# Performance work log

Measured on AMD Instinct MI355X. Metric: run time of the kernel, lower is better.

The kernel has to match this reference:

```python
import jax, jax.numpy as jnp
import numpy as np


def setup_inputs() -> dict:
    key = jax.random.key(0)
    k1, k2 = jax.random.split(key)
    B, S, H, T = 32, 524288, 512, 100
    n_frames = S // H  # 1024
    wrapped_phase = jax.random.uniform(k1, (B, S), dtype=jnp.float32)  # in [0,1)
    tables = jax.random.normal(k2, (B, n_frames + 1, T), dtype=jnp.float32)
    return {"wrapped_phase": wrapped_phase, "tables": tables, "hop_length": H}


def reference(wrapped_phase, tables, hop_length):
    # wrapped_phase: (B, S) in [0,1]; tables: (B, n_frames+1, T); hop_length: python int
    B, S = wrapped_phase.shape
    H = hop_length
    pad = (-S) % H
    wp = jnp.pad(wrapped_phase, ((0, 0), (0, pad)), mode="edge")
    wp = wp.reshape(B, -1, H)          # (B, F, H)
    Fr = wp.shape[1]
    if tables.shape[1] < Fr + 1:
        tables = jnp.pad(tables, ((0, 0), (0, Fr + 1 - tables.shape[1]), (0, 0)), mode="edge")
    else:
        tables = tables[:, : Fr + 1]
    L = tables.shape[2]
    # bilinear interp along table axis
    raw = wp * L                                   # (B, F, H)
    floor = jnp.clip(raw.astype(jnp.int32), 0, L - 1)
    p = raw - floor.astype(wp.dtype)
    # wrap-around pad: append first table entry at the end
    padded = jnp.concatenate([tables, tables[:, :, :1]], axis=2)  # (B, F+1, L+1)
    floor_flow = padded[:, :-1]   # table at frame start
    ceil_flow = padded[:, 1:]     # table at next frame

    def gather(t, idx):
        return jnp.take_along_axis(t, idx, axis=2)  # (B, F, H)

    v_floor = gather(floor_flow, floor) * (1.0 - p) + gather(floor_flow, floor + 1) * p
    v_ceil = gather(ceil_flow, floor) * (1.0 - p) + gather(ceil_flow, floor + 1) * p
    # lerp across hop-time
    p2 = jnp.arange(H, dtype=wp.dtype) / H          # (H,)
    final = v_floor * (1.0 - p2) + v_ceil * p2      # (B, F, H)
    return final.reshape(B, -1)[:, :S]
```

## Files before the change

### kernel.cpp

```cpp
#include <hip/hip_runtime.h>

constexpr int Bc  = 32;
constexpr int Sc  = 524288;
constexpr int Hc  = 512;
constexpr int Tc  = 100;
constexpr int FRc = Sc / Hc;
constexpr int FPB = 2;
constexpr int THREADS = 256;

typedef float floatx4 __attribute__((ext_vector_type(4)));

__global__ __launch_bounds__(THREADS) void gft_kernel(
    const float* __restrict__ wp,
    const float* __restrict__ tables,
    float* __restrict__ out)
{
    __shared__ floatx4 pk[FPB][Tc];

    const int blk = blockIdx.x;
    const int b   = blk >> 9;
    const int fp  = blk & 511;
    const int f   = fp * FPB;
    const int t   = threadIdx.x;

    const size_t base = (size_t)b * Sc + (size_t)fp * (FPB * Hc) + (size_t)t * 4;
    const floatx4 w = __builtin_nontemporal_load(
        reinterpret_cast<const floatx4*>(wp + base));

    const float* trow = tables + ((size_t)b * (FRc + 1) + (size_t)f) * Tc;
    if (t < FPB * Tc) {
        const int fr = (t >= Tc) ? 1 : 0;
        const int i  = t - fr * Tc;
        const int i1 = (i == Tc - 1) ? 0 : i + 1;
        const float* F = trow + fr * Tc;
        const float* C = F + Tc;
        floatx4 v;
        v.x = F[i]; v.y = F[i1]; v.z = C[i]; v.w = C[i1];
        pk[fr][i] = v;
    }
    __syncthreads();

    const int fi = t >> 7;
    const int h0 = (t & 127) * 4;

    const float wv[4] = {w.x, w.y, w.z, w.w};
    float r[4];
    #pragma unroll
    for (int j = 0; j < 4; ++j) {
        float raw = wv[j] * (float)Tc;
        int   fl  = (int)raw;
        fl = fl < 0 ? 0 : (fl > Tc - 1 ? Tc - 1 : fl);
        float p   = raw - (float)fl;
        float omp = 1.0f - p;
        floatx4 g = pk[fi][fl];
        float vf  = g.x * omp + g.y * p;
        float vc  = g.z * omp + g.w * p;
        float p2  = (float)(h0 + j) * (1.0f / (float)Hc);
        r[j] = vf * (1.0f - p2) + vc * p2;
    }
    floatx4 res;
    res.x = r[0]; res.y = r[1]; res.z = r[2]; res.w = r[3];
    __builtin_nontemporal_store(res, reinterpret_cast<floatx4*>(out + base));
}

extern "C" void kernel_launch(void* const* d_in, const int* in_sizes, int n_in,
                              void* d_out, int out_size, void* d_ws, size_t ws_size,
                              hipStream_t stream) {
    const float* wp     = (const float*)d_in[0];
    const float* tables = (const float*)d_in[1];
    float*       out    = (float*)d_out;
    gft_kernel<<<dim3(Bc * (FRc / FPB)), dim3(THREADS), 0, stream>>>(wp, tables, out);
}
```

Measured before the change: 28.26 us.

## Assign one frame per wavefront and drop block-wide barrier

Each 64-lane wavefront now owns a whole frame: it builds that frame's packed table in shared memory and then interpolates 8 samples per lane, so no __syncthreads is needed. Blocks cover 4 frames instead of 2, which halves the grid size and doubles per-thread work and memory-level parallelism. This relies on wavefront-synchronous execution (64 lanes) for the shared-memory writes to be visible to reads in the same wave, with no explicit barrier or fence.

After: 28.62 us. About the same (+1.3%).

```diff
diff --git a/kernel.cpp b/kernel.cpp
--- a/kernel.cpp
+++ b/kernel.cpp
@@ -5,7 +5,7 @@
 constexpr int Hc  = 512;
 constexpr int Tc  = 100;
 constexpr int FRc = Sc / Hc;
-constexpr int FPB = 2;
+constexpr int FPB = 4;
 constexpr int THREADS = 256;
 
 typedef float floatx4 __attribute__((ext_vector_type(4)));
@@ -17,50 +17,63 @@
 {
     __shared__ floatx4 pk[FPB][Tc];
 
-    const int blk = blockIdx.x;
-    const int b   = blk >> 9;
-    const int fp  = blk & 511;
-    const int f   = fp * FPB;
-    const int t   = threadIdx.x;
+    const int blk  = blockIdx.x;
+    const int b    = blk >> 8;
+    const int g    = blk & 255;
+    const int t    = threadIdx.x;
+    const int wave = t >> 6;
+    const int lane = t & 63;
+    const int f    = g * FPB + wave;
 
-    const size_t base = (size_t)b * Sc + (size_t)fp * (FPB * Hc) + (size_t)t * 4;
-    const floatx4 w = __builtin_nontemporal_load(
-        reinterpret_cast<const floatx4*>(wp + base));
+    const size_t fbase = (size_t)b * Sc + (size_t)f * Hc;
+    const floatx4 w0 = __builtin_nontemporal_load(
+        reinterpret_cast<const floatx4*>(wp + fbase + (size_t)lane * 4));
+    const floatx4 w1 = __builtin_nontemporal_load(
+        reinterpret_cast<const floatx4*>(wp + fbase + 256 + (size_t)lane * 4));
 
     const float* trow = tables + ((size_t)b * (FRc + 1) + (size_t)f) * Tc;
-    if (t < FPB * Tc) {
-        const int fr = (t >= Tc) ? 1 : 0;
-        const int i  = t - fr * Tc;
-        const int i1 = (i == Tc - 1) ? 0 : i + 1;
-        const float* F = trow + fr * Tc;
-        const float* C = F + Tc;
+    {
+        const int e  = lane;
+        const int e1 = e + 1;
         floatx4 v;
-        v.x = F[i]; v.y = F[i1]; v.z = C[i]; v.w = C[i1];
-        pk[fr][i] = v;
+        v.x = trow[e];  v.y = trow[e1];
+        v.z = trow[Tc + e]; v.w = trow[Tc + e1];
+        pk[wave][e] = v;
     }
-    __syncthreads();
+    if (lane < Tc - 64) {
+        const int e  = 64 + lane;
+        const int e1 = (e == Tc - 1) ? 0 : e + 1;
+        floatx4 v;
+        v.x = trow[e];  v.y = trow[e1];
+        v.z = trow[Tc + e]; v.w = trow[Tc + e1];
+        pk[wave][e] = v;
+    }
 
-    const int fi = t >> 7;
-    const int h0 = (t & 127) * 4;
-
-    const float wv[4] = {w.x, w.y, w.z, w.w};
-    float r[4];
+    const float wv[8] = {w0.x, w0.y, w0.z, w0.w, w1.x, w1.y, w1.z, w1.w};
+    float r[8];
     #pragma unroll
-    for (int j = 0; j < 4; ++j) {
-        float raw = wv[j] * (float)Tc;
+    for (int s = 0; s < 8; ++s) {
+        const int c = s >> 2, j = s & 3;
+        const int h = c * 256 + lane * 4 + j;
+        float raw = wv[s] * (float)Tc;
         int   fl  = (int)raw;
         fl = fl < 0 ? 0 : (fl > Tc - 1 ? Tc - 1 : fl);
         float p   = raw - (float)fl;
         float omp = 1.0f - p;
-        floatx4 g = pk[fi][fl];
-        float vf  = g.x * omp + g.y * p;
-        float vc  = g.z * omp + g.w * p;
-        float p2  = (float)(h0 + j) * (1.0f / (float)Hc);
-        r[j] = vf * (1.0f - p2) + vc * p2;
+        floatx4 gv = pk[wave][fl];
+        float vf  = gv.x * omp + gv.y * p;
+        float vc  = gv.z * omp + gv.w * p;
+        float p2  = (float)h * (1.0f / (float)Hc);
+        r[s] = vf * (1.0f - p2) + vc * p2;
     }
-    floatx4 res;
-    res.x = r[0]; res.y = r[1]; res.z = r[2]; res.w = r[3];
-    __builtin_nontemporal_store(res, reinterpret_cast<floatx4*>(out + base));
+
+    floatx4 o0, o1;
+    o0.x = r[0]; o0.y = r[1]; o0.z = r[2]; o0.w = r[3];
+    o1.x = r[4]; o1.y = r[5]; o1.z = r[6]; o1.w = r[7];
+    __builtin_nontemporal_store(o0,
+        reinterpret_cast<floatx4*>(out + fbase + (size_t)lane * 4));
+    __builtin_nontemporal_store(o1,
+        reinterpret_cast<floatx4*>(out + fbase + 256 + (size_t)lane * 4));
 }
 
 extern "C" void kernel_launch(void* const* d_in, const int* in_sizes, int n_in,
```
